# Kernel tuning notes

Measured on AMD Instinct MI355X. Metric: run time of the kernel, lower is better.

Reference implementation:

```python
import jax, jax.numpy as jnp
import numpy as np

TREE_DEPTH = 6
NUM_TREES = 64
NUM_LEAVES = 2 ** TREE_DEPTH
INPUT_DIM = 256
BATCH = 32768
BN_EPS = 1e-5


def _leaf_codes():
    # [L, depth] binary codes, MSB first (matches format(i, '0{depth}b'))
    i = np.arange(NUM_LEAVES)
    bits = (i[:, None] >> np.arange(TREE_DEPTH - 1, -1, -1)[None, :]) & 1
    return jnp.asarray(bits, dtype=jnp.float32)


def setup_inputs() -> dict:
    key = jax.random.key(0)
    ks = jax.random.split(key, 6)
    s = 1.0 / np.sqrt(INPUT_DIM)
    return {
        "x": jax.random.normal(ks[0], (BATCH, INPUT_DIM), jnp.float32),
        "W_dec": jax.random.normal(ks[1], (NUM_TREES, TREE_DEPTH, INPUT_DIM), jnp.float32) * s,
        "b_dec": jax.random.normal(ks[2], (NUM_TREES, TREE_DEPTH), jnp.float32) * s,
        "leaf_values": jax.random.normal(ks[3], (NUM_TREES, NUM_LEAVES), jnp.float32),
        "bn_gamma": jnp.ones((NUM_TREES,), jnp.float32),
        "bn_beta": jnp.zeros((NUM_TREES,), jnp.float32),
        "bn_mean": jnp.zeros((NUM_TREES,), jnp.float32),
        "bn_var": jnp.ones((NUM_TREES,), jnp.float32),
        "fc_w": jax.random.normal(ks[4], (INPUT_DIM, NUM_TREES), jnp.float32) / np.sqrt(NUM_TREES),
        "fc_b": jnp.zeros((INPUT_DIM,), jnp.float32),
    }


def reference(x, W_dec, b_dec, leaf_values, bn_gamma, bn_beta, bn_mean, bn_var, fc_w, fc_b):
    # Decision probabilities for all trees at once: [B, T, depth]
    dec = jax.nn.sigmoid(jnp.einsum("bd,tkd->btk", x, W_dec) + b_dec)
    codes = _leaf_codes()  # [L, depth]
    # Leaf probabilities: product over depth of (dec*code + (1-dec)*(1-code)).
    # Loop over the small fixed depth to avoid a [B,T,L,depth] intermediate.
    probs = jnp.ones((x.shape[0], NUM_TREES, NUM_LEAVES), x.dtype)
    for d in range(TREE_DEPTH):
        dd = dec[:, :, d][:, :, None]            # [B, T, 1]
        c = codes[:, d]                          # [L]
        probs = probs * (dd * c + (1.0 - dd) * (1.0 - c))
    # Weighted sum of leaf values per tree: [B, T]
    tree_out = jnp.einsum("btl,tl->bt", probs, leaf_values)
    # BatchNorm1d in eval mode (running stats), dropout is identity in eval.
    tree_out = (tree_out - bn_mean) * jax.lax.rsqrt(bn_var + BN_EPS) * bn_gamma + bn_beta
    # Final projection back to input_dim: [B, D]
    return tree_out @ fc_w.T + fc_b
```

## Files before the change

kernel.cpp:

```cpp
#include <hip/hip_runtime.h>

typedef __attribute__((ext_vector_type(8))) short short8;
typedef __attribute__((ext_vector_type(4))) float floatx4;

#define LOG2E 1.4426950408889634f

__device__ __forceinline__ unsigned short f2bf(float f) {
  unsigned int u = __float_as_uint(f);
  u += 0x7FFFu + ((u >> 16) & 1u);
  return (unsigned short)(u >> 16);
}

__global__ void prep_kernel(const float* __restrict__ W_dec,
                            const float* __restrict__ b_dec,
                            const float* __restrict__ leaf,
                            const float* __restrict__ bn_gamma,
                            const float* __restrict__ bn_beta,
                            const float* __restrict__ bn_mean,
                            const float* __restrict__ bn_var,
                            const float* __restrict__ fc_w,
                            unsigned short* __restrict__ Wp,
                            unsigned short* __restrict__ fcw,
                            float* __restrict__ leaf2,
                            float* __restrict__ b1,
                            float* __restrict__ sb,
                            float* __restrict__ ob)
{
  int idx = (int)blockIdx.x * 256 + (int)threadIdx.x;
  if (idx < 384 * 256) {
    int np = idx >> 8, k = idx & 255;
    int d = np >> 6, t = np & 63;
    Wp[idx] = f2bf(-LOG2E * W_dec[(t * 6 + d) * 256 + k]);
    return;
  }
  idx -= 384 * 256;
  if (idx < 256 * 64) { fcw[idx] = f2bf(fc_w[idx]); return; }
  idx -= 256 * 64;
  if (idx < 2048) {
    int t = idx >> 5, i = idx & 31;
    float a = leaf[t * 64 + 2 * i];
    float b = leaf[t * 64 + 2 * i + 1];
    leaf2[t * 64 + 2 * i]     = a;
    leaf2[t * 64 + 2 * i + 1] = b - a;
    return;
  }
  idx -= 2048;
  if (idx < 384) {
    int t = idx / 6, d = idx % 6;
    b1[d * 64 + t] = -LOG2E * b_dec[idx];
    return;
  }
  idx -= 384;
  if (idx < 64) {
    float s = bn_gamma[idx] * rsqrtf(bn_var[idx] + 1e-5f);
    sb[idx] = s;
    ob[idx] = bn_beta[idx] - bn_mean[idx] * s;
  }
}

__global__ __launch_bounds__(256, 2)
void node_main(const float* __restrict__ x,
               const unsigned short* __restrict__ Wp,
               const unsigned short* __restrict__ fcw,
               const float* __restrict__ leaf2,
               const float* __restrict__ b1g,
               const float* __restrict__ sbg,
               const float* __restrict__ obg,
               const float* __restrict__ fc_b,
               float* __restrict__ out)
{
  __shared__ unsigned short A_lds[64][264];
  __shared__ float leaf_lds[64][68];
  __shared__ unsigned short A2_lds[64][72];
  __shared__ float b1_lds[384];
  __shared__ float sb_lds[64];
  __shared__ float ob_lds[64];
  __shared__ float fcb_lds[256];

  const int tid  = (int)threadIdx.x;
  const int lane = tid & 63;
  const int w    = tid >> 6;
  const int tcol = lane & 15;
  const int g    = lane >> 4;
  const int r0   = (int)blockIdx.x * 64;

  {
    const float4* xs = (const float4*)(x + (size_t)r0 * 256);
    #pragma unroll
    for (int i = 0; i < 16; ++i) {
      int f = tid + 256 * i;
      float4 v = xs[f];
      int row = f >> 6, c4 = f & 63;
      unsigned int lo = (unsigned int)f2bf(v.x) | ((unsigned int)f2bf(v.y) << 16);
      unsigned int hi = (unsigned int)f2bf(v.z) | ((unsigned int)f2bf(v.w) << 16);
      unsigned int* p = (unsigned int*)&A_lds[row][c4 * 4];
      p[0] = lo; p[1] = hi;
    }
    #pragma unroll
    for (int i = 0; i < 4; ++i) {
      int f = tid + 256 * i;
      float4 v = ((const float4*)leaf2)[f];
      int t = f >> 4, c4 = f & 15;
      *(float4*)&leaf_lds[t][c4 * 4] = v;
    }
    b1_lds[tid] = b1g[tid];
    if (tid < 128) b1_lds[256 + tid] = b1g[256 + tid];
    if (tid < 64) { sb_lds[tid] = sbg[tid]; ob_lds[tid] = obg[tid]; }
    fcb_lds[tid] = fc_b[tid];
  }
  __syncthreads();

  floatx4 acc[4][6];
  #pragma unroll
  for (int rt = 0; rt < 4; ++rt)
    #pragma unroll
    for (int d = 0; d < 6; ++d) { acc[rt][d][0]=0.f; acc[rt][d][1]=0.f; acc[rt][d][2]=0.f; acc[rt][d][3]=0.f; }

  const unsigned short* Bb = Wp + (size_t)(w * 16 + tcol) * 256 + g * 8;

  short8 bA[6], bB[6];
  #pragma unroll
  for (int d = 0; d < 6; ++d) bA[d] = *(const short8*)(Bb + d * 16384);

  #pragma unroll 1
  for (int kp = 0; kp < 4; ++kp) {
    #pragma unroll
    for (int d = 0; d < 6; ++d) bB[d] = *(const short8*)(Bb + d * 16384 + (kp * 2 + 1) * 32);
    short8 a[4];
    #pragma unroll
    for (int rt = 0; rt < 4; ++rt)
      a[rt] = *(const short8*)&A_lds[rt * 16 + tcol][kp * 64 + g * 8];
    #pragma unroll
    for (int d = 0; d < 6; ++d)
      #pragma unroll
      for (int rt = 0; rt < 4; ++rt)
        acc[rt][d] = __builtin_amdgcn_mfma_f32_16x16x32_bf16(a[rt], bA[d], acc[rt][d], 0, 0, 0);
    if (kp < 3) {
      #pragma unroll
      for (int d = 0; d < 6; ++d) bA[d] = *(const short8*)(Bb + d * 16384 + (kp * 2 + 2) * 32);
    }
    #pragma unroll
    for (int rt = 0; rt < 4; ++rt)
      a[rt] = *(const short8*)&A_lds[rt * 16 + tcol][kp * 64 + 32 + g * 8];
    #pragma unroll
    for (int d = 0; d < 6; ++d)
      #pragma unroll
      for (int rt = 0; rt < 4; ++rt)
        acc[rt][d] = __builtin_amdgcn_mfma_f32_16x16x32_bf16(a[rt], bB[d], acc[rt][d], 0, 0, 0);
  }

  const int tree = w * 16 + tcol;
  float bp[6];
  #pragma unroll
  for (int d = 0; d < 6; ++d) bp[d] = b1_lds[d * 64 + tree];
  const float sbv = sb_lds[tree], obv = ob_lds[tree];

  #pragma unroll
  for (int rt = 0; rt < 4; ++rt)
    #pragma unroll
    for (int d = 0; d < 6; ++d)
      #pragma unroll
      for (int j = 0; j < 4; ++j) {
        float z = acc[rt][d][j] + bp[d];
        acc[rt][d][j] = __builtin_amdgcn_rcpf(1.0f + __builtin_amdgcn_exp2f(z));
      }

  float L[32], resLo[16];
  #pragma unroll
  for (int c = 0; c < 8; ++c) {
    float4 v = *(const float4*)&leaf_lds[tree][c * 4];
    L[c*4+0] = v.x; L[c*4+1] = v.y; L[c*4+2] = v.z; L[c*4+3] = v.w;
  }
  #pragma unroll
  for (int rt = 0; rt < 4; ++rt)
    #pragma unroll
    for (int j = 0; j < 4; ++j) {
      float u[16];
      const float d5 = acc[rt][5][j];
      #pragma unroll
      for (int i = 0; i < 16; ++i) u[i] = fmaf(d5, L[2*i+1], L[2*i]);
      const float d4 = acc[rt][4][j];
      #pragma unroll
      for (int i = 0; i < 8; ++i) u[i] = fmaf(d4, u[2*i+1] - u[2*i], u[2*i]);
      const float d3 = acc[rt][3][j];
      #pragma unroll
      for (int i = 0; i < 4; ++i) u[i] = fmaf(d3, u[2*i+1] - u[2*i], u[2*i]);
      const float d2 = acc[rt][2][j];
      #pragma unroll
      for (int i = 0; i < 2; ++i) u[i] = fmaf(d2, u[2*i+1] - u[2*i], u[2*i]);
      resLo[rt*4+j] = fmaf(acc[rt][1][j], u[1] - u[0], u[0]);
    }
  #pragma unroll
  for (int c = 0; c < 8; ++c) {
    float4 v = *(const float4*)&leaf_lds[tree][32 + c * 4];
    L[c*4+0] = v.x; L[c*4+1] = v.y; L[c*4+2] = v.z; L[c*4+3] = v.w;
  }
  #pragma unroll
  for (int rt = 0; rt < 4; ++rt)
    #pragma unroll
    for (int j = 0; j < 4; ++j) {
      float u[16];
      const float d5 = acc[rt][5][j];
      #pragma unroll
      for (int i = 0; i < 16; ++i) u[i] = fmaf(d5, L[2*i+1], L[2*i]);
      const float d4 = acc[rt][4][j];
      #pragma unroll
      for (int i = 0; i < 8; ++i) u[i] = fmaf(d4, u[2*i+1] - u[2*i], u[2*i]);
      const float d3 = acc[rt][3][j];
      #pragma unroll
      for (int i = 0; i < 4; ++i) u[i] = fmaf(d3, u[2*i+1] - u[2*i], u[2*i]);
      const float d2 = acc[rt][2][j];
      #pragma unroll
      for (int i = 0; i < 2; ++i) u[i] = fmaf(d2, u[2*i+1] - u[2*i], u[2*i]);
      float hi_r = fmaf(acc[rt][1][j], u[1] - u[0], u[0]);
      float lo_r = resLo[rt*4+j];
      float to   = fmaf(acc[rt][0][j], hi_r - lo_r, lo_r);
      float vv   = fmaf(to, sbv, obv);
      A2_lds[rt * 16 + g * 4 + j][tree] = f2bf(vv);
    }
  __syncthreads();

  floatx4 acc2[4][4];
  #pragma unroll
  for (int rt = 0; rt < 4; ++rt)
    #pragma unroll
    for (int nt = 0; nt < 4; ++nt) { acc2[rt][nt][0]=0.f; acc2[rt][nt][1]=0.f; acc2[rt][nt][2]=0.f; acc2[rt][nt][3]=0.f; }

  #pragma unroll
  for (int kst = 0; kst < 2; ++kst) {
    short8 a2[4];
    #pragma unroll
    for (int rt = 0; rt < 4; ++rt)
      a2[rt] = *(const short8*)&A2_lds[rt * 16 + tcol][kst * 32 + g * 8];
    #pragma unroll
    for (int nt = 0; nt < 4; ++nt) {
      short8 b2 = *(const short8*)(fcw + (size_t)(w * 64 + nt * 16 + tcol) * 64 + kst * 32 + g * 8);
      #pragma unroll
      for (int rt = 0; rt < 4; ++rt)
        acc2[rt][nt] = __builtin_amdgcn_mfma_f32_16x16x32_bf16(a2[rt], b2, acc2[rt][nt], 0, 0, 0);
    }
  }

  #pragma unroll
  for (int nt = 0; nt < 4; ++nt) {
    const int col = w * 64 + nt * 16 + tcol;
    const float bv = fcb_lds[col];
    #pragma unroll
    for (int rt = 0; rt < 4; ++rt)
      #pragma unroll
      for (int j = 0; j < 4; ++j)
        out[(size_t)(r0 + rt * 16 + g * 4 + j) * 256 + col] = acc2[rt][nt][j] + bv;
  }
}

extern "C" void kernel_launch(void* const* d_in, const int* in_sizes, int n_in,
                              void* d_out, int out_size, void* d_ws, size_t ws_size,
                              hipStream_t stream) {
  const float* x        = (const float*)d_in[0];
  const float* W_dec    = (const float*)d_in[1];
  const float* b_dec    = (const float*)d_in[2];
  const float* leaf     = (const float*)d_in[3];
  const float* bn_gamma = (const float*)d_in[4];
  const float* bn_beta  = (const float*)d_in[5];
  const float* bn_mean  = (const float*)d_in[6];
  const float* bn_var   = (const float*)d_in[7];
  const float* fc_w     = (const float*)d_in[8];
  const float* fc_b     = (const float*)d_in[9];
  float* out = (float*)d_out;

  char* ws = (char*)d_ws;
  unsigned short* Wp  = (unsigned short*)(ws);
  unsigned short* fcw = (unsigned short*)(ws + 196608);
  float* leaf2 = (float*)(ws + 229376);
  float* b1    = (float*)(ws + 245760);
  float* sb    = (float*)(ws + 247296);
  float* ob    = (float*)(ws + 247552);

  prep_kernel<<<458, 256, 0, stream>>>(W_dec, b_dec, leaf, bn_gamma, bn_beta,
                                       bn_mean, bn_var, fc_w,
                                       Wp, fcw, leaf2, b1, sb, ob);
  node_main<<<512, 256, 0, stream>>>(x, Wp, fcw, leaf2, b1, sb, ob, fc_b, out);
}
```

Baseline: 38.81 us.

## Use multilinear leaf coefficients, stream x directly into MFMA, halve block rows

The leaf values are turned into multilinear polynomial coefficients in the prep kernel, with the BatchNorm scale and offset folded in. The per-level reduction then becomes a single FMA per node, with no subtraction, and the separate BN step is dropped. The main kernel no longer stages x in LDS: each lane loads fp32 x directly from global and packs it to bf16 for the MFMA operand. Rows per block drop from 64 to 32, with twice as many blocks and a higher launch-bounds occupancy target. The risk is uncoalesced, unreused global reads of x and higher bandwidth pressure on the fp32 input.

```diff
diff --git a/kernel.cpp b/kernel.cpp
--- a/kernel.cpp
+++ b/kernel.cpp
@@ -1,4 +1,5 @@
 #include <hip/hip_runtime.h>
+#include <hip/hip_bf16.h>
 
 typedef __attribute__((ext_vector_type(8))) short short8;
 typedef __attribute__((ext_vector_type(4))) float floatx4;
@@ -9,6 +10,22 @@
   unsigned int u = __float_as_uint(f);
   u += 0x7FFFu + ((u >> 16) & 1u);
   return (unsigned short)(u >> 16);
+}
+
+__device__ __forceinline__ unsigned int pk2(float lo, float hi) {
+  __hip_bfloat162 h = __float22bfloat162_rn(make_float2(lo, hi));
+  unsigned int u;
+  __builtin_memcpy(&u, &h, 4);
+  return u;
+}
+
+__device__ __forceinline__ short8 pack8(float4 a, float4 b) {
+  union { unsigned int u[4]; short8 s; } r;
+  r.u[0] = pk2(a.x, a.y);
+  r.u[1] = pk2(a.z, a.w);
+  r.u[2] = pk2(b.x, b.y);
+  r.u[3] = pk2(b.z, b.w);
+  return r.s;
 }
 
 __global__ void prep_kernel(const float* __restrict__ W_dec,
@@ -21,10 +38,8 @@
                             const float* __restrict__ fc_w,
                             unsigned short* __restrict__ Wp,
                             unsigned short* __restrict__ fcw,
-                            float* __restrict__ leaf2,
-                            float* __restrict__ b1,
-                            float* __restrict__ sb,
-                            float* __restrict__ ob)
+                            float* __restrict__ coefg,
+                            float* __restrict__ b1)
 {
   int idx = (int)blockIdx.x * 256 + (int)threadIdx.x;
   if (idx < 384 * 256) {
@@ -36,45 +51,46 @@
   idx -= 384 * 256;
   if (idx < 256 * 64) { fcw[idx] = f2bf(fc_w[idx]); return; }
   idx -= 256 * 64;
-  if (idx < 2048) {
-    int t = idx >> 5, i = idx & 31;
-    float a = leaf[t * 64 + 2 * i];
-    float b = leaf[t * 64 + 2 * i + 1];
-    leaf2[t * 64 + 2 * i]     = a;
-    leaf2[t * 64 + 2 * i + 1] = b - a;
+  if (idx < 64) {
+    const int t = idx;
+    float c[64];
+    #pragma unroll
+    for (int i = 0; i < 64; ++i) c[i] = leaf[t * 64 + i];
+    #pragma unroll
+    for (int p = 0; p < 6; ++p) {
+      const int s = 1 << p;
+      #pragma unroll
+      for (int i = 0; i < 64; ++i)
+        if ((i & s) == 0) c[i + s] -= c[i];
+    }
+    float sbv = bn_gamma[t] * rsqrtf(bn_var[t] + 1e-5f);
+    float obv = bn_beta[t] - bn_mean[t] * sbv;
+    #pragma unroll
+    for (int i = 0; i < 64; ++i) c[i] *= sbv;
+    c[0] += obv;
+    #pragma unroll
+    for (int i = 0; i < 64; ++i) coefg[t * 64 + i] = c[i];
     return;
   }
-  idx -= 2048;
+  idx -= 64;
   if (idx < 384) {
     int t = idx / 6, d = idx % 6;
     b1[d * 64 + t] = -LOG2E * b_dec[idx];
-    return;
-  }
-  idx -= 384;
-  if (idx < 64) {
-    float s = bn_gamma[idx] * rsqrtf(bn_var[idx] + 1e-5f);
-    sb[idx] = s;
-    ob[idx] = bn_beta[idx] - bn_mean[idx] * s;
-  }
-}
-
-__global__ __launch_bounds__(256, 2)
+  }
+}
+
+__global__ __launch_bounds__(256, 4)
 void node_main(const float* __restrict__ x,
                const unsigned short* __restrict__ Wp,
                const unsigned short* __restrict__ fcw,
-               const float* __restrict__ leaf2,
+               const float* __restrict__ coefg,
                const float* __restrict__ b1g,
-               const float* __restrict__ sbg,
-               const float* __restrict__ obg,
                const float* __restrict__ fc_b,
                float* __restrict__ out)
 {
-  __shared__ unsigned short A_lds[64][264];
-  __shared__ float leaf_lds[64][68];
-  __shared__ unsigned short A2_lds[64][72];
+  __shared__ float coef_lds[64][68];
+  __shared__ unsigned short A2_lds[32][72];
   __shared__ float b1_lds[384];
-  __shared__ float sb_lds[64];
-  __shared__ float ob_lds[64];
   __shared__ float fcb_lds[256];
 
   const int tid  = (int)threadIdx.x;
@@ -82,81 +98,55 @@
   const int w    = tid >> 6;
   const int tcol = lane & 15;
   const int g    = lane >> 4;
-  const int r0   = (int)blockIdx.x * 64;
-
-  {
-    const float4* xs = (const float4*)(x + (size_t)r0 * 256);
-    #pragma unroll
-    for (int i = 0; i < 16; ++i) {
-      int f = tid + 256 * i;
-      float4 v = xs[f];
-      int row = f >> 6, c4 = f & 63;
-      unsigned int lo = (unsigned int)f2bf(v.x) | ((unsigned int)f2bf(v.y) << 16);
-      unsigned int hi = (unsigned int)f2bf(v.z) | ((unsigned int)f2bf(v.w) << 16);
-      unsigned int* p = (unsigned int*)&A_lds[row][c4 * 4];
-      p[0] = lo; p[1] = hi;
-    }
-    #pragma unroll
-    for (int i = 0; i < 4; ++i) {
-      int f = tid + 256 * i;
-      float4 v = ((const float4*)leaf2)[f];
-      int t = f >> 4, c4 = f & 15;
-      *(float4*)&leaf_lds[t][c4 * 4] = v;
-    }
-    b1_lds[tid] = b1g[tid];
-    if (tid < 128) b1_lds[256 + tid] = b1g[256 + tid];
-    if (tid < 64) { sb_lds[tid] = sbg[tid]; ob_lds[tid] = obg[tid]; }
-    fcb_lds[tid] = fc_b[tid];
+  const int r0   = (int)blockIdx.x * 32;
+
+  #pragma unroll
+  for (int i = 0; i < 4; ++i) {
+    int f = tid + 256 * i;
+    int t = f >> 4, c4 = f & 15;
+    *(float4*)&coef_lds[t][c4 * 4] = ((const float4*)coefg)[f];
+  }
+  b1_lds[tid] = b1g[tid];
+  if (tid < 128) b1_lds[256 + tid] = b1g[256 + tid];
+  fcb_lds[tid] = fc_b[tid];
+
+  floatx4 acc[2][6];
+  #pragma unroll
+  for (int rt = 0; rt < 2; ++rt)
+    #pragma unroll
+    for (int d = 0; d < 6; ++d) { acc[rt][d][0]=0.f; acc[rt][d][1]=0.f; acc[rt][d][2]=0.f; acc[rt][d][3]=0.f; }
+
+  const unsigned short* Bb = Wp + (size_t)(w * 16 + tcol) * 256 + g * 8;
+  const float* Ab = x + (size_t)(r0 + tcol) * 256 + g * 8;
+
+  #pragma unroll 2
+  for (int kp = 0; kp < 8; ++kp) {
+    short8 b[6];
+    #pragma unroll
+    for (int d = 0; d < 6; ++d) b[d] = *(const short8*)(Bb + d * 16384 + kp * 32);
+    short8 a[2];
+    #pragma unroll
+    for (int rt = 0; rt < 2; ++rt) {
+      const float* p = Ab + rt * 16 * 256 + kp * 32;
+      float4 v0 = *(const float4*)p;
+      float4 v1 = *(const float4*)(p + 4);
+      a[rt] = pack8(v0, v1);
+    }
+    #pragma unroll
+    for (int d = 0; d < 6; ++d)
+      #pragma unroll
+      for (int rt = 0; rt < 2; ++rt)
+        acc[rt][d] = __builtin_amdgcn_mfma_f32_16x16x32_bf16(a[rt], b[d], acc[rt][d], 0, 0, 0);
   }
   __syncthreads();
-
-  floatx4 acc[4][6];
-  #pragma unroll
-  for (int rt = 0; rt < 4; ++rt)
-    #pragma unroll
-    for (int d = 0; d < 6; ++d) { acc[rt][d][0]=0.f; acc[rt][d][1]=0.f; acc[rt][d][2]=0.f; acc[rt][d][3]=0.f; }
-
-  const unsigned short* Bb = Wp + (size_t)(w * 16 + tcol) * 256 + g * 8;
-
-  short8 bA[6], bB[6];
-  #pragma unroll
-  for (int d = 0; d < 6; ++d) bA[d] = *(const short8*)(Bb + d * 16384);
-
-  #pragma unroll 1
-  for (int kp = 0; kp < 4; ++kp) {
-    #pragma unroll
-    for (int d = 0; d < 6; ++d) bB[d] = *(const short8*)(Bb + d * 16384 + (kp * 2 + 1) * 32);
-    short8 a[4];
-    #pragma unroll
-    for (int rt = 0; rt < 4; ++rt)
-      a[rt] = *(const short8*)&A_lds[rt * 16 + tcol][kp * 64 + g * 8];
-    #pragma unroll
-    for (int d = 0; d < 6; ++d)
-      #pragma unroll
-      for (int rt = 0; rt < 4; ++rt)
-        acc[rt][d] = __builtin_amdgcn_mfma_f32_16x16x32_bf16(a[rt], bA[d], acc[rt][d], 0, 0, 0);
-    if (kp < 3) {
-      #pragma unroll
-      for (int d = 0; d < 6; ++d) bA[d] = *(const short8*)(Bb + d * 16384 + (kp * 2 + 2) * 32);
-    }
-    #pragma unroll
-    for (int rt = 0; rt < 4; ++rt)
-      a[rt] = *(const short8*)&A_lds[rt * 16 + tcol][kp * 64 + 32 + g * 8];
-    #pragma unroll
-    for (int d = 0; d < 6; ++d)
-      #pragma unroll
-      for (int rt = 0; rt < 4; ++rt)
-        acc[rt][d] = __builtin_amdgcn_mfma_f32_16x16x32_bf16(a[rt], bB[d], acc[rt][d], 0, 0, 0);
-  }
 
   const int tree = w * 16 + tcol;
   float bp[6];
   #pragma unroll
   for (int d = 0; d < 6; ++d) bp[d] = b1_lds[d * 64 + tree];
-  const float sbv = sb_lds[tree], obv = ob_lds[tree];
-
-  #pragma unroll
-  for (int rt = 0; rt < 4; ++rt)
+
+  #pragma unroll
+  for (int rt = 0; rt < 2; ++rt)
     #pragma unroll
     for (int d = 0; d < 6; ++d)
       #pragma unroll
@@ -165,14 +155,14 @@
         acc[rt][d][j] = __builtin_amdgcn_rcpf(1.0f + __builtin_amdgcn_exp2f(z));
       }
 
-  float L[32], resLo[16];
+  float L[32], resLo[8];
   #pragma unroll
   for (int c = 0; c < 8; ++c) {
-    float4 v = *(const float4*)&leaf_lds[tree][c * 4];
+    float4 v = *(const float4*)&coef_lds[tree][c * 4];
     L[c*4+0] = v.x; L[c*4+1] = v.y; L[c*4+2] = v.z; L[c*4+3] = v.w;
   }
   #pragma unroll
-  for (int rt = 0; rt < 4; ++rt)
+  for (int rt = 0; rt < 2; ++rt)
     #pragma unroll
     for (int j = 0; j < 4; ++j) {
       float u[16];
@@ -181,22 +171,22 @@
       for (int i = 0; i < 16; ++i) u[i] = fmaf(d5, L[2*i+1], L[2*i]);
       const float d4 = acc[rt][4][j];
       #pragma unroll
-      for (int i = 0; i < 8; ++i) u[i] = fmaf(d4, u[2*i+1] - u[2*i], u[2*i]);
+      for (int i = 0; i < 8; ++i) u[i] = fmaf(d4, u[2*i+1], u[2*i]);
       const float d3 = acc[rt][3][j];
       #pragma unroll
-      for (int i = 0; i < 4; ++i) u[i] = fmaf(d3, u[2*i+1] - u[2*i], u[2*i]);
+      for (int i = 0; i < 4; ++i) u[i] = fmaf(d3, u[2*i+1], u[2*i]);
       const float d2 = acc[rt][2][j];
       #pragma unroll
-      for (int i = 0; i < 2; ++i) u[i] = fmaf(d2, u[2*i+1] - u[2*i], u[2*i]);
-      resLo[rt*4+j] = fmaf(acc[rt][1][j], u[1] - u[0], u[0]);
+      for (int i = 0; i < 2; ++i) u[i] = fmaf(d2, u[2*i+1], u[2*i]);
+      resLo[rt*4+j] = fmaf(acc[rt][1][j], u[1], u[0]);
     }
   #pragma unroll
   for (int c = 0; c < 8; ++c) {
-    float4 v = *(const float4*)&leaf_lds[tree][32 + c * 4];
+    float4 v = *(const float4*)&coef_lds[tree][32 + c * 4];
     L[c*4+0] = v.x; L[c*4+1] = v.y; L[c*4+2] = v.z; L[c*4+3] = v.w;
   }
   #pragma unroll
-  for (int rt = 0; rt < 4; ++rt)
+  for (int rt = 0; rt < 2; ++rt)
     #pragma unroll
     for (int j = 0; j < 4; ++j) {
       float u[16];
@@ -205,38 +195,36 @@
       for (int i = 0; i < 16; ++i) u[i] = fmaf(d5, L[2*i+1], L[2*i]);
       const float d4 = acc[rt][4][j];
       #pragma unroll
-      for (int i = 0; i < 8; ++i) u[i] = fmaf(d4, u[2*i+1] - u[2*i], u[2*i]);
+      for (int i = 0; i < 8; ++i) u[i] = fmaf(d4, u[2*i+1], u[2*i]);
       const float d3 = acc[rt][3][j];
       #pragma unroll
-      for (int i = 0; i < 4; ++i) u[i] = fmaf(d3, u[2*i+1] - u[2*i], u[2*i]);
+      for (int i = 0; i < 4; ++i) u[i] = fmaf(d3, u[2*i+1], u[2*i]);
       const float d2 = acc[rt][2][j];
       #pragma unroll
-      for (int i = 0; i < 2; ++i) u[i] = fmaf(d2, u[2*i+1] - u[2*i], u[2*i]);
-      float hi_r = fmaf(acc[rt][1][j], u[1] - u[0], u[0]);
-      float lo_r = resLo[rt*4+j];
-      float to   = fmaf(acc[rt][0][j], hi_r - lo_r, lo_r);
-      float vv   = fmaf(to, sbv, obv);
-      A2_lds[rt * 16 + g * 4 + j][tree] = f2bf(vv);
+      for (int i = 0; i < 2; ++i) u[i] = fmaf(d2, u[2*i+1], u[2*i]);
+      float hi_r = fmaf(acc[rt][1][j], u[1], u[0]);
+      float to   = fmaf(acc[rt][0][j], hi_r, resLo[rt*4+j]);
+      A2_lds[rt * 16 + g * 4 + j][tree] = f2bf(to);
     }
   __syncthreads();
 
-  floatx4 acc2[4][4];
-  #pragma unroll
-  for (int rt = 0; rt < 4; ++rt)
+  floatx4 acc2[2][4];
+  #pragma unroll
+  for (int rt = 0; rt < 2; ++rt)
     #pragma unroll
     for (int nt = 0; nt < 4; ++nt) { acc2[rt][nt][0]=0.f; acc2[rt][nt][1]=0.f; acc2[rt][nt][2]=0.f; acc2[rt][nt][3]=0.f; }
 
   #pragma unroll
   for (int kst = 0; kst < 2; ++kst) {
-    short8 a2[4];
-    #pragma unroll
-    for (int rt = 0; rt < 4; ++rt)
+    short8 a2[2];
+    #pragma unroll
+    for (int rt = 0; rt < 2; ++rt)
       a2[rt] = *(const short8*)&A2_lds[rt * 16 + tcol][kst * 32 + g * 8];
     #pragma unroll
     for (int nt = 0; nt < 4; ++nt) {
       short8 b2 = *(const short8*)(fcw + (size_t)(w * 64 + nt * 16 + tcol) * 64 + kst * 32 + g * 8);
       #pragma unroll
-      for (int rt = 0; rt < 4; ++rt)
+      for (int rt = 0; rt < 2; ++rt)
         acc2[rt][nt] = __builtin_amdgcn_mfma_f32_16x16x32_bf16(a2[rt], b2, acc2[rt][nt], 0, 0, 0);
     }
   }
@@ -246,7 +234,7 @@
     const int col = w * 64 + nt * 16 + tcol;
     const float bv = fcb_lds[col];
     #pragma unroll
-    for (int rt = 0; rt < 4; ++rt)
+    for (int rt = 0; rt < 2; ++rt)
       #pragma unroll
       for (int j = 0; j < 4; ++j)
         out[(size_t)(r0 + rt * 16 + g * 4 + j) * 256 + col] = acc2[rt][nt][j] + bv;
@@ -271,13 +259,11 @@
   char* ws = (char*)d_ws;
   unsigned short* Wp  = (unsigned short*)(ws);
   unsigned short* fcw = (unsigned short*)(ws + 196608);
-  float* leaf2 = (float*)(ws + 229376);
+  float* coefg = (float*)(ws + 229376);
   float* b1    = (float*)(ws + 245760);
-  float* sb    = (float*)(ws + 247296);
-  float* ob    = (float*)(ws + 247552);
-
-  prep_kernel<<<458, 256, 0, stream>>>(W_dec, b_dec, leaf, bn_gamma, bn_beta,
+
+  prep_kernel<<<450, 256, 0, stream>>>(W_dec, b_dec, leaf, bn_gamma, bn_beta,
                                        bn_mean, bn_var, fc_w,
-                                       Wp, fcw, leaf2, b1, sb, ob);
-  node_main<<<512, 256, 0, stream>>>(x, Wp, fcw, leaf2, b1, sb, ob, fc_b, out);
-}
+                                       Wp, fcw, coefg, b1);
+  node_main<<<1024, 256, 0, stream>>>(x, Wp, fcw, coefg, b1, fc_b, out);
+}
```

Measured after the change: 56.69 us. 1.46x slower.
